# Performance work log

Hardware: AMD Instinct MI355X
Metric: run time of the kernel (lower is better)

The kernel has to match this reference:

```python
import jax, jax.numpy as jnp
import numpy as np

SOGLIA = 0.333
# db4 analysis lowpass filter stored time-reversed (= rec_lo scaling filter), matching
# pytorch_wavelets prep_filt_afb1d (weight = dec_lo[::-1]) used with cross-correlation.
DB4_H = np.array([0.23037781330885523, 0.7148465705525415, 0.6308807679295904,
                  -0.02798376941698385, -0.18703481171888114, 0.030841381835986965,
                  0.032883011666982945, -0.010597401784997278], dtype=np.float32)


def dwt_lo(x):
    # Single-level DWT lowpass with mode='zero' (pytorch_wavelets afb1d semantics).
    # x: (B, N, D), filtering + stride-2 downsample along token axis N.
    B, N, D = x.shape
    L = DB4_H.shape[0]
    outsize = (N + L - 1) // 2            # pywt.dwt_coeff_len for zero mode
    p = 2 * (outsize - 1) - N + L         # total pad needed
    if p % 2 == 1:                        # odd: extra zero at the end first
        x = jnp.pad(x, ((0, 0), (0, 1), (0, 0)))
    x = jnp.pad(x, ((0, 0), (p // 2, p // 2), (0, 0)))
    k = jnp.tile(jnp.asarray(DB4_H, x.dtype)[None, None, :], (D, 1, 1))  # (D,1,L) depthwise
    y = jax.lax.conv_general_dilated(x.transpose(0, 2, 1), k, window_strides=(2,),
                                     padding='VALID', feature_group_count=D)
    return y.transpose(0, 2, 1)           # (B, outsize, D)


def compute_gini(probs):
    B, N = probs.shape
    sp = jnp.sort(probs, axis=1)
    idx = jnp.arange(1, N + 1, dtype=sp.dtype)
    return 2.0 * (idx * sp).sum(axis=1) / (N * sp.sum(axis=1) + 1e-8) - (N + 1) / N


def setup_inputs() -> dict:
    key = jax.random.key(0)
    k1, k2 = jax.random.split(key)
    x = jax.random.normal(k1, (256, 197, 768), dtype=jnp.float32)
    cls_attention_map = jax.random.uniform(k2, (256, 196), dtype=jnp.float32)
    return {"x": x, "cls_attention_map": cls_attention_map}


def reference(x, cls_attention_map):
    B, N, D = x.shape
    cls_tok, patch = x[:, :1], x[:, 1:]            # (B,1,D), (B,N-1,D)
    gini = compute_gini(cls_attention_map)
    level2 = gini > SOGLIA                         # route: True -> J=2, False -> J=1
    y1 = dwt_lo(patch)                             # level-1 lowpass (B, len1, D)
    y2 = dwt_lo(y1)                                # level-2 lowpass (B, len2, D)
    len1, len2 = y1.shape[1], y2.shape[1]
    y2p = jnp.pad(y2, ((0, 0), (0, len1 - len2), (0, 0)))
    final_patches = jnp.where(level2[:, None, None], y2p, y1)   # dense-expert combine
    out_len = jnp.where(level2, len2, len1)
    final_x = jnp.concatenate([cls_tok, final_patches], axis=1)  # (B, len1+1, D)
    mask = jnp.arange(len1)[None, :] < out_len[:, None]
    mask = jnp.concatenate([jnp.ones((B, 1), dtype=bool), mask], axis=1)
    return final_x, mask
```

## Files before the change

kernel.cpp:

```cpp
#include <hip/hip_runtime.h>

#define NB   256
#define NTOK 197
#define NP   196
#define ND   768
#define LEN1 101
#define LEN2 54
#define OUTROWS 102
#define NGRP 51
#define NWG  (NB * NGRP)

typedef float f4 __attribute__((ext_vector_type(4)));

__global__ __launch_bounds__(256)
void gini_kernel(const float* __restrict__ attn, int* __restrict__ flags) {
    __shared__ float  row[NP];
    __shared__ double sS[256];
    __shared__ double sT[256];
    const int b   = blockIdx.x;
    const int tid = threadIdx.x;
    if (tid < NP) row[tid] = attn[b * NP + tid];
    __syncthreads();
    double sj = 0.0, tj = 0.0;
    if (tid < NP) {
        const float p = row[tid];
        int rank = 1;
        for (int k = 0; k < NP; ++k) {
            const float q = row[k];
            rank += (q < p) || (q == p && k < tid);
        }
        sj = (double)rank * (double)p;
        tj = (double)p;
    }
    sS[tid] = sj; sT[tid] = tj;
    __syncthreads();
    for (int off = 128; off > 0; off >>= 1) {
        if (tid < off) { sS[tid] += sS[tid + off]; sT[tid] += sT[tid + off]; }
        __syncthreads();
    }
    if (tid == 0) {
        const double S = sS[0], T = sT[0];
        const double gini = 2.0 * S / ((double)NP * T + 1e-8)
                          - (double)(NP + 1) / (double)NP;
        flags[b] = (gini > (double)0.333f) ? 1 : 0;
    }
}

__global__ __launch_bounds__(192)
void dwt_kernel(const float* __restrict__ x, const int* __restrict__ flags,
                float* __restrict__ out_x, float* __restrict__ out_mask) {
    const float h[8] = {0.23037781330885523f,  0.7148465705525415f,
                        0.6308807679295904f,  -0.02798376941698385f,
                       -0.18703481171888114f,  0.030841381835986965f,
                        0.032883011666982945f,-0.010597401784997278f};
    float g2[22];
    #pragma unroll
    for (int m = 0; m < 22; ++m) {
        float s = 0.f;
        #pragma unroll
        for (int j = 0; j < 8; ++j) {
            const int l = m - 2 * j;
            if (0 <= l && l < 8) s += h[j] * h[l];
        }
        g2[m] = s;
    }

    const int hw  = blockIdx.x;
    const int per = NWG / 8;
    const int bid = (hw & 7) * per + (hw >> 3);
    const int b   = bid / NGRP;
    const int grp = bid - b * NGRP;
    const int c   = threadIdx.x;
    const int d0  = c * 4;

    const float* __restrict__ px = x + ((size_t)b * NTOK + 1) * ND + d0;
    float* __restrict__ po = out_x + (size_t)b * OUTROWS * ND + d0;
    const int flag = flags[b];

    auto raw = [&](int i) -> f4 { return *(const f4*)(px + (size_t)i * ND); };
    auto clamped = [&](int i) -> f4 {
        return (i >= 0 && i < NP) ? *(const f4*)(px + (size_t)i * ND)
                                  : (f4){0.f, 0.f, 0.f, 0.f};
    };

    if (grp == 0) {
        const f4 cls = *(const f4*)(x + (size_t)b * NTOK * ND + d0);
        __builtin_nontemporal_store(cls, (f4*)po);
        if (c < OUTROWS) {
            const int outlen = flag ? LEN2 : LEN1;
            out_mask[b * OUTROWS + c] = (c == 0 || (c - 1) < outlen) ? 1.0f : 0.0f;
        }
        f4 y = {0.f, 0.f, 0.f, 0.f};
        if (!flag) {
            y += h[6] * clamped(0);
            y += h[7] * clamped(1);
        } else {
            #pragma unroll
            for (int m = 18; m < 22; ++m) y += g2[m] * clamped(m - 18);
        }
        __builtin_nontemporal_store(y, (f4*)(po + (size_t)ND));
        return;
    }

    if (!flag) {
        const int lo = 4 * grp - 8;
        f4 w[10];
        if (grp >= 2 && grp <= 48) {
            #pragma unroll
            for (int k = 0; k < 10; ++k) w[k] = raw(lo + k);
        } else {
            #pragma unroll
            for (int k = 0; k < 10; ++k) w[k] = clamped(lo + k);
        }
        f4 y0 = {0.f,0.f,0.f,0.f}, y1 = {0.f,0.f,0.f,0.f};
        #pragma unroll
        for (int l = 0; l < 8; ++l) {
            y0 += h[l] * w[l];
            y1 += h[l] * w[l + 2];
        }
        __builtin_nontemporal_store(y0, (f4*)(po + (size_t)(2 * grp) * ND));
        __builtin_nontemporal_store(y1, (f4*)(po + (size_t)(2 * grp + 1) * ND));
    } else {
        const int s0 = 2 * grp - 1;
        if (s0 < LEN2) {
            const int lo = 8 * grp - 22;
            f4 y0 = {0.f,0.f,0.f,0.f}, y1 = {0.f,0.f,0.f,0.f};
            auto run = [&](auto ld) {
                {
                    f4 w[13];
                    #pragma unroll
                    for (int j = 0; j < 13; ++j) w[j] = ld(lo + j);
                    #pragma unroll
                    for (int j = 0; j < 13; ++j) {
                        y0 += g2[j] * w[j];
                        if (j >= 4) y1 += g2[j - 4] * w[j];
                    }
                }
                {
                    f4 w[13];
                    #pragma unroll
                    for (int j = 0; j < 13; ++j) w[j] = ld(lo + 13 + j);
                    #pragma unroll
                    for (int j = 0; j < 13; ++j) {
                        if (13 + j < 22) y0 += g2[13 + j] * w[j];
                        y1 += g2[9 + j] * w[j];
                    }
                }
            };
            if (grp >= 3 && grp <= 24) run(raw); else run(clamped);
            if (s0 + 1 >= LEN2) y1 = (f4){0.f,0.f,0.f,0.f};
            __builtin_nontemporal_store(y0, (f4*)(po + (size_t)(2 * grp) * ND));
            __builtin_nontemporal_store(y1, (f4*)(po + (size_t)(2 * grp + 1) * ND));
        } else {
            const f4 zero = {0.f,0.f,0.f,0.f};
            __builtin_nontemporal_store(zero, (f4*)(po + (size_t)(2 * grp) * ND));
            __builtin_nontemporal_store(zero, (f4*)(po + (size_t)(2 * grp + 1) * ND));
        }
    }
}

extern "C" void kernel_launch(void* const* d_in, const int* in_sizes, int n_in,
                              void* d_out, int out_size, void* d_ws, size_t ws_size,
                              hipStream_t stream) {
    const float* x    = (const float*)d_in[0];
    const float* attn = (const float*)d_in[1];
    float* out_x    = (float*)d_out;
    float* out_mask = (float*)d_out + (size_t)NB * OUTROWS * ND;
    int* flags = (int*)d_ws;

    gini_kernel<<<NB, 256, 0, stream>>>(attn, flags);
    dwt_kernel<<<NWG, 192, 0, stream>>>(x, flags, out_x, out_mask);
}
```

Baseline: 44.69 us.

## Fuse gini routing computation into DWT kernel, dropping the separate launch

Removes the standalone gini kernel and has every DWT workgroup recompute the gini coefficient for its batch row from the attention map. It uses shared memory, a vectorized rank count and a wavefront shuffle reduction. This eliminates a kernel launch and the global flag round trip between the two stages. The cost is redundant O(N^2) rank computation in each of the 51 workgroups per batch, plus two barriers before the streaming loads start.

```diff
diff --git a/kernel.cpp b/kernel.cpp
--- a/kernel.cpp
+++ b/kernel.cpp
@@ -12,43 +12,9 @@
 
 typedef float f4 __attribute__((ext_vector_type(4)));
 
-__global__ __launch_bounds__(256)
-void gini_kernel(const float* __restrict__ attn, int* __restrict__ flags) {
-    __shared__ float  row[NP];
-    __shared__ double sS[256];
-    __shared__ double sT[256];
-    const int b   = blockIdx.x;
-    const int tid = threadIdx.x;
-    if (tid < NP) row[tid] = attn[b * NP + tid];
-    __syncthreads();
-    double sj = 0.0, tj = 0.0;
-    if (tid < NP) {
-        const float p = row[tid];
-        int rank = 1;
-        for (int k = 0; k < NP; ++k) {
-            const float q = row[k];
-            rank += (q < p) || (q == p && k < tid);
-        }
-        sj = (double)rank * (double)p;
-        tj = (double)p;
-    }
-    sS[tid] = sj; sT[tid] = tj;
-    __syncthreads();
-    for (int off = 128; off > 0; off >>= 1) {
-        if (tid < off) { sS[tid] += sS[tid + off]; sT[tid] += sT[tid + off]; }
-        __syncthreads();
-    }
-    if (tid == 0) {
-        const double S = sS[0], T = sT[0];
-        const double gini = 2.0 * S / ((double)NP * T + 1e-8)
-                          - (double)(NP + 1) / (double)NP;
-        flags[b] = (gini > (double)0.333f) ? 1 : 0;
-    }
-}
-
 __global__ __launch_bounds__(192)
-void dwt_kernel(const float* __restrict__ x, const int* __restrict__ flags,
-                float* __restrict__ out_x, float* __restrict__ out_mask) {
+void fused_kernel(const float* __restrict__ x, const float* __restrict__ attn,
+                  float* __restrict__ out_x, float* __restrict__ out_mask) {
     const float h[8] = {0.23037781330885523f,  0.7148465705525415f,
                         0.6308807679295904f,  -0.02798376941698385f,
                        -0.18703481171888114f,  0.030841381835986965f,
@@ -73,9 +39,53 @@
     const int c   = threadIdx.x;
     const int d0  = c * 4;
 
+    __shared__ __align__(16) float arow[NP];
+    __shared__ double redS[3], redT[3];
+    __shared__ int    sflag;
+    if (c < NP / 4) *(f4*)&arow[4 * c] = *(const f4*)(attn + (size_t)b * NP + 4 * c);
+    __syncthreads();
+    {
+        double sj = 0.0, tj = 0.0;
+        #pragma unroll
+        for (int rep = 0; rep < 2; ++rep) {
+            const int i = c + rep * 192;
+            if (i < NP) {
+                const float p = arow[i];
+                int rank = 1;
+                for (int k4 = 0; k4 < NP / 4; ++k4) {
+                    const f4 qv = *(const f4*)&arow[4 * k4];
+                    #pragma unroll
+                    for (int e = 0; e < 4; ++e) {
+                        const float qe = qv[e];
+                        const int idx = 4 * k4 + e;
+                        rank += (qe < p) || (qe == p && idx < i);
+                    }
+                }
+                sj += (double)rank * (double)p;
+                tj += (double)p;
+            }
+        }
+        #pragma unroll
+        for (int off = 32; off > 0; off >>= 1) {
+            sj += __shfl_down(sj, off);
+            tj += __shfl_down(tj, off);
+        }
+        const int wid = c >> 6, lane = c & 63;
+        if (lane == 0) { redS[wid] = sj; redT[wid] = tj; }
+        __syncthreads();
+        if (c == 0) {
+            const double S = redS[0] + redS[1] + redS[2];
+            const double T = redT[0] + redT[1] + redT[2];
+            const double gini = 2.0 * S / ((double)NP * T + 1e-8)
+                              - (double)(NP + 1) / (double)NP;
+            sflag = (gini > (double)0.333f) ? 1 : 0;
+        }
+        __syncthreads();
+    }
+    const int flag = sflag;
+
     const float* __restrict__ px = x + ((size_t)b * NTOK + 1) * ND + d0;
     float* __restrict__ po = out_x + (size_t)b * OUTROWS * ND + d0;
-    const int flag = flags[b];
 
     auto raw = [&](int i) -> f4 { return *(const f4*)(px + (size_t)i * ND); };
     auto clamped = [&](int i) -> f4 {
@@ -166,8 +176,6 @@
     const float* attn = (const float*)d_in[1];
     float* out_x    = (float*)d_out;
     float* out_mask = (float*)d_out + (size_t)NB * OUTROWS * ND;
-    int* flags = (int*)d_ws;
 
-    gini_kernel<<<NB, 256, 0, stream>>>(attn, flags);
-    dwt_kernel<<<NWG, 192, 0, stream>>>(x, flags, out_x, out_mask);
+    fused_kernel<<<NWG, 192, 0, stream>>>(x, attn, out_x, out_mask);
 }
```

Result: slower. 137.4 us (+207.4%).
